# Optimization experiments

Hardware: AMD Instinct MI355X
Metric: run time of the kernel (lower is better)

## Reference

```python
import jax, jax.numpy as jnp
import numpy as np

B, GH, GW, DIM, NH = 1, 48, 64, 1536, 16
HD = DIM // NH          # 96
C = HD // 2             # 48, divisible by 3 as the rope split requires
L = max(GH, GW)


def setup_inputs() -> dict:
    key = jax.random.key(0)
    ks = jax.random.split(key, 6)
    x = jax.random.normal(ks[0], (B, GH * GW, DIM), jnp.float32)
    w_init = lambda k: jax.random.normal(k, (DIM, DIM), jnp.float32) * 0.02
    # rope frequency table: theta[p, j] = p / 10000^(j/C); freqs = exp(i*theta)
    pos = jnp.arange(L, dtype=jnp.float32)[:, None]
    inv = 10000.0 ** (-jnp.arange(C, dtype=jnp.float32) / C)
    theta = pos * inv[None, :]
    return {
        "x": x,
        "wq": w_init(ks[1]), "bq": jnp.zeros((DIM,), jnp.float32),
        "wk": w_init(ks[2]), "bk": jnp.zeros((DIM,), jnp.float32),
        "wv": w_init(ks[3]), "bv": jnp.zeros((DIM,), jnp.float32),
        "wo": w_init(ks[4]), "bo": jnp.zeros((DIM,), jnp.float32),
        "freqs_cos": jnp.cos(theta), "freqs_sin": jnp.sin(theta),
        "h": GH, "w": GW,
    }


def rope_apply_spatial(x, freqs_cos, freqs_sin, h, w):
    # x: [b, s, n, d] with s == h*w. Complex rotation done in real arithmetic.
    b, s, n, d = x.shape
    c = d // 2
    c3 = c // 3
    # channel groups: [0:c3] identity (ones), [c3:2c3] rotated by h-position,
    # [2c3:3c3] rotated by w-position  (matches freqs.split + cat in torch)
    cos_hw = jnp.concatenate([
        jnp.ones((h, w, c3), x.dtype),
        jnp.broadcast_to(freqs_cos[:h, None, c3:2 * c3], (h, w, c3)),
        jnp.broadcast_to(freqs_cos[None, :w, 2 * c3:3 * c3], (h, w, c3)),
    ], axis=-1).reshape(1, s, 1, c)
    sin_hw = jnp.concatenate([
        jnp.zeros((h, w, c3), x.dtype),
        jnp.broadcast_to(freqs_sin[:h, None, c3:2 * c3], (h, w, c3)),
        jnp.broadcast_to(freqs_sin[None, :w, 2 * c3:3 * c3], (h, w, c3)),
    ], axis=-1).reshape(1, s, 1, c)
    xc = x.reshape(b, s, n, c, 2)
    xr, xi = xc[..., 0], xc[..., 1]
    yr = xr * cos_hw - xi * sin_hw
    yi = xr * sin_hw + xi * cos_hw
    return jnp.stack([yr, yi], axis=-1).reshape(b, s, n, d)


def reference(x, wq, bq, wk, bk, wv, bv, wo, bo, freqs_cos, freqs_sin, h, w):
    b, s, _ = x.shape
    q = (x @ wq + bq).reshape(b, s, NH, HD)
    k = (x @ wk + bk).reshape(b, s, NH, HD)
    v = (x @ wv + bv).reshape(b, s, NH, HD)
    q = rope_apply_spatial(q, freqs_cos, freqs_sin, h, w)
    k = rope_apply_spatial(k, freqs_cos, freqs_sin, h, w)
    scale = 1.0 / jnp.sqrt(jnp.asarray(HD, q.dtype))
    scores = jnp.einsum('bqnd,bknd->bnqk', q, k) * scale  # [b, n, s, s]
    attn = jax.nn.softmax(scores, axis=-1)
    out = jnp.einsum('bnqk,bknd->bqnd', attn, v).reshape(b, s, NH * HD)
    return out @ wo + bo
```

## Files before the change

kernel.cpp:

```cpp
#include <hip/hip_runtime.h>
#include <math.h>

#define S_LEN 3072
#define DIM 1536
#define NHEADS 16
#define HDIM 96
#define NPAIR 48

typedef __attribute__((ext_vector_type(8))) _Float16 half8;
typedef __attribute__((ext_vector_type(4))) _Float16 half4v;
typedef __attribute__((ext_vector_type(2))) _Float16 half2v;
typedef __attribute__((ext_vector_type(4))) float f32x4;

__device__ inline void gload16(const void* g, void* l) {
    __builtin_amdgcn_global_load_lds(
        (const __attribute__((address_space(1))) void*)g,
        (__attribute__((address_space(3))) void*)l, 16, 0, 0);
}

__device__ inline uint4 gld128(const _Float16* p) {
    uint4 r;
    asm volatile("global_load_dwordx4 %0, %1, off"
                 : "=v"(r) : "v"(p));
    return r;
}

__global__ __launch_bounds__(256)
void convert_f32_f16(const float* __restrict__ src, _Float16* __restrict__ dst, int n4)
{
    int i = blockIdx.x * 256 + threadIdx.x;
    if (i < n4) {
        float4 v = *(const float4*)&src[(size_t)i * 4];
        half4v h = { (_Float16)v.x, (_Float16)v.y, (_Float16)v.z, (_Float16)v.w };
        *(half4v*)&dst[(size_t)i * 4] = h;
    }
}

__global__ __launch_bounds__(256)
void transpose_w(const float* __restrict__ w0, const float* __restrict__ w1,
                 const float* __restrict__ w2, const float* __restrict__ w3,
                 _Float16* __restrict__ wt)
{
    __shared__ _Float16 t[64][68];
    const int z = blockIdx.z;
    const float* W = (z == 0) ? w0 : (z == 1) ? w1 : (z == 2) ? w2 : w3;
    _Float16* O = wt + (size_t)z * DIM * DIM;
    const int k0 = blockIdx.y * 64, n0 = blockIdx.x * 64;
    const int tid = threadIdx.x;
    const int r = tid >> 4, c4 = (tid & 15) * 4;
#pragma unroll
    for (int g = 0; g < 4; g++) {
        int kk = r + g * 16;
        float4 v = *(const float4*)&W[(size_t)(k0 + kk) * DIM + n0 + c4];
        t[c4 + 0][kk] = (_Float16)v.x; t[c4 + 1][kk] = (_Float16)v.y;
        t[c4 + 2][kk] = (_Float16)v.z; t[c4 + 3][kk] = (_Float16)v.w;
    }
    __syncthreads();
    const int nr = tid >> 2, ks = (tid & 3) * 16;
#pragma unroll
    for (int s = 0; s < 4; s++)
        *(ushort4*)&O[(size_t)(n0 + nr) * DIM + k0 + ks + s * 4] =
            *(ushort4*)&t[nr][ks + s * 4];
}

template<bool QKV>
__global__ __launch_bounds__(256)
void gemm_f16(const _Float16* __restrict__ X,
              const _Float16* __restrict__ W0t, const _Float16* __restrict__ W1t,
              const _Float16* __restrict__ W2t,
              const float* __restrict__ B0, const float* __restrict__ B1,
              const float* __restrict__ B2,
              const float* __restrict__ fc, const float* __restrict__ fs,
              void* __restrict__ outv)
{
    __shared__ __align__(16) _Float16 As[128][64];
    __shared__ __align__(16) _Float16 Bs[128][64];

    const int tid = threadIdx.x;
    const int w = tid >> 6, lane = tid & 63;
    const int ln = lane & 15, quad = lane >> 4;
    const int bz = blockIdx.z;
    const _Float16* Wt = W0t; const float* bias = B0;
    if (QKV) { if (bz == 1) { Wt = W1t; bias = B1; } else if (bz == 2) { Wt = W2t; bias = B2; } }
    const int m0 = blockIdx.y * 128, n0 = blockIdx.x * 128;
    const int wm = w >> 1, wn = w & 1;
    const int row8 = lane >> 3, cch = lane & 7;
    const int gch = cch ^ row8;

    f32x4 acc[4][4];
#pragma unroll
    for (int i = 0; i < 4; i++)
#pragma unroll
        for (int j = 0; j < 4; j++) acc[i][j] = (f32x4){0.f, 0.f, 0.f, 0.f};

    for (int k0 = 0; k0 < DIM; k0 += 64) {
        __syncthreads();
#pragma unroll
        for (int j = 0; j < 4; j++) {
            const int r = w * 32 + j * 8;
            gload16(X  + (size_t)(m0 + r + row8) * DIM + k0 + gch * 8, &As[r][0]);
            gload16(Wt + (size_t)(n0 + r + row8) * DIM + k0 + gch * 8, &Bs[r][0]);
        }
        __syncthreads();

        half8 a[4][2], b[4][2];
#pragma unroll
        for (int mt = 0; mt < 4; mt++) {
            int m = wm * 64 + mt * 16 + ln;
#pragma unroll
            for (int ks = 0; ks < 2; ks++) {
                int s = (ks * 4 + quad) ^ (ln & 7);
                a[mt][ks] = *(const half8*)&As[m][s * 8];
            }
        }
#pragma unroll
        for (int nt = 0; nt < 4; nt++) {
            int n = wn * 64 + nt * 16 + ln;
#pragma unroll
            for (int ks = 0; ks < 2; ks++) {
                int s = (ks * 4 + quad) ^ (ln & 7);
                b[nt][ks] = *(const half8*)&Bs[n][s * 8];
            }
        }
#pragma unroll
        for (int ks = 0; ks < 2; ks++)
#pragma unroll
            for (int mt = 0; mt < 4; mt++)
#pragma unroll
                for (int nt = 0; nt < 4; nt++)
                    acc[mt][nt] = __builtin_amdgcn_mfma_f32_16x16x32_f16(
                        a[mt][ks], b[nt][ks], acc[mt][nt], 0, 0, 0);
    }

#pragma unroll
    for (int nt = 0; nt < 4; nt++) {
        int col = n0 + wn * 64 + nt * 16 + ln;
        float bv = bias[col];
        int head = col / HDIM, hd = col % HDIM;
        int jc = hd >> 1;
        bool isreal = (ln & 1) == 0;
#pragma unroll
        for (int mt = 0; mt < 4; mt++) {
            int row0 = m0 + wm * 64 + mt * 16 + quad * 4;
            if (QKV && bz == 2) {
                half4v p;
#pragma unroll
                for (int r = 0; r < 4; r++) p[r] = (_Float16)(acc[mt][nt][r] + bv);
                *(half4v*)&((_Float16*)outv)[(((size_t)2 * NHEADS + head) * HDIM + hd) * S_LEN + row0] = p;
            } else if (QKV) {
                float v[4], vp[4];
#pragma unroll
                for (int r = 0; r < 4; r++) v[r] = acc[mt][nt][r] + bv;
#pragma unroll
                for (int r = 0; r < 4; r++) vp[r] = __shfl_xor(v[r], 1);
#pragma unroll
                for (int r = 0; r < 4; r++) {
                    int srow = row0 + r;
                    int pos = (jc < 32) ? (srow >> 6) : (srow & 63);
                    float c  = fc[pos * NPAIR + jc];
                    float sn = fs[pos * NPAIR + jc];
                    float xr = isreal ? v[r] : vp[r];
                    float xi = isreal ? vp[r] : v[r];
                    float rot = isreal ? (xr * c - xi * sn) : (xr * sn + xi * c);
                    float outval = (jc < 16) ? v[r] : rot;
                    ((_Float16*)outv)[(((size_t)bz * NHEADS + head) * S_LEN + srow) * HDIM + hd]
                        = (_Float16)outval;
                }
            } else {
#pragma unroll
                for (int r = 0; r < 4; r++)
                    ((float*)outv)[(size_t)(row0 + r) * DIM + col] = acc[mt][nt][r] + bv;
            }
        }
    }
}

__global__ __launch_bounds__(256, 2)
void attn_mfma_kernel(const _Float16* __restrict__ qh, const _Float16* __restrict__ kh,
                      const _Float16* __restrict__ vtg, _Float16* __restrict__ aoh)
{
    __shared__ __align__(16) _Float16 Kb[2][2][64 * 96];
    __shared__ __align__(16) _Float16 Vt[2][96][72];

    const int tid  = threadIdx.x;
    const int wid  = tid >> 6;
    const int p    = wid >> 1;
    const int wp   = wid & 1;
    const int lane = tid & 63;
    const int ln   = lane & 15;
    const int quad = lane >> 4;
    const int h    = blockIdx.y;
    const int q0   = blockIdx.x * 64;
    const float scale_ = 0.10206207261596577f * 1.4426950408889634f;
    const int NT = (S_LEN / 2) / 64;

    half8 aq[2][3];
#pragma unroll
    for (int qs = 0; qs < 2; qs++) {
        const _Float16* qrow = qh + (((size_t)h * S_LEN) + q0 + (wp * 2 + qs) * 16 + ln) * HDIM;
#pragma unroll
        for (int kb = 0; kb < 3; kb++) {
            half8 a = *(const half8*)&qrow[kb * 32 + quad * 8];
            half8 v;
#pragma unroll
            for (int i = 0; i < 8; i++) v[i] = (_Float16)((float)a[i] * scale_);
            aq[qs][kb] = v;
        }
    }

    f32x4 o[2][6];
#pragma unroll
    for (int qs = 0; qs < 2; qs++)
#pragma unroll
        for (int dn = 0; dn < 6; dn++) o[qs][dn] = (f32x4){0.f, 0.f, 0.f, 0.f};
    float m_[2] = {-INFINITY, -INFINITY}, l_[2] = {0.f, 0.f};

    const char* kbase = (const char*)(kh + ((size_t)h * S_LEN + p * (S_LEN / 2)) * HDIM);

    int koffb[6];
#pragma unroll
    for (int i = 0; i < 6; i++) {
        int pc = i * 128 + (tid & 127);
        int r  = pc / 12, c = pc - r * 12;
        int rm = r % 12;
        int cl = c - rm; if (cl < 0) cl += 12;
        koffb[i] = r * 192 + cl * 16;
    }
    const int A0 = (quad + ln) % 12;
    int ksel[3];
    ksel[0] = A0 * 16;
    { int t1 = A0 + 4; if (t1 >= 12) t1 -= 12; ksel[1] = t1 * 16; }
    { int t2 = A0 + 8; if (t2 >= 12) t2 -= 12; ksel[2] = t2 * 16; }

    const int tp = tid & 127;
    const int vd0 = tp >> 3, vc = tp & 7;
    const _Float16* vsrc0 = vtg + (size_t)h * HDIM * S_LEN + (size_t)vd0 * S_LEN
                          + p * (S_LEN / 2) + vc * 8;
    _Float16* vdst = &Vt[p][vd0][(vc ^ (vd0 & 7)) * 8];

#pragma unroll
    for (int i = 0; i < 6; i++)
        gload16(kbase + koffb[i], &Kb[p][0][i * 1024 + wp * 512]);
    uint4 vp0, vp1, vp2, vp3, vp4, vp5;
    vp0 = gld128(vsrc0 + 0 * 16 * S_LEN);
    vp1 = gld128(vsrc0 + 1 * 16 * S_LEN);
    vp2 = gld128(vsrc0 + 2 * 16 * S_LEN);
    vp3 = gld128(vsrc0 + 3 * 16 * S_LEN);
    vp4 = gld128(vsrc0 + 4 * 16 * S_LEN);
    vp5 = gld128(vsrc0 + 5 * 16 * S_LEN);
    asm volatile("s_waitcnt vmcnt(0)" ::: "memory");
    __builtin_amdgcn_sched_barrier(0);
    *(uint4*)(vdst + 0 * 16 * 72) = vp0;  *(uint4*)(vdst + 1 * 16 * 72) = vp1;
    *(uint4*)(vdst + 2 * 16 * 72) = vp2;  *(uint4*)(vdst + 3 * 16 * 72) = vp3;
    *(uint4*)(vdst + 4 * 16 * 72) = vp4;  *(uint4*)(vdst + 5 * 16 * 72) = vp5;
    __syncthreads();

    for (int kt = 0; kt < NT; ++kt) {
        const int cur = kt & 1;
        if (kt + 1 < NT) {
            const char* ks2 = kbase + (size_t)(kt + 1) * 12288;
#pragma unroll
            for (int i = 0; i < 6; i++)
                gload16(ks2 + koffb[i], &Kb[p][cur ^ 1][i * 1024 + wp * 512]);
            const _Float16* vs2 = vsrc0 + (kt + 1) * 64;
            vp0 = gld128(vs2 + 0 * 16 * S_LEN);
            vp1 = gld128(vs2 + 1 * 16 * S_LEN);
            vp2 = gld128(vs2 + 2 * 16 * S_LEN);
            vp3 = gld128(vs2 + 3 * 16 * S_LEN);
            vp4 = gld128(vs2 + 4 * 16 * S_LEN);
            vp5 = gld128(vs2 + 5 * 16 * S_LEN);
            __builtin_amdgcn_sched_barrier(0);
        }

        const char* Kc = (const char*)&Kb[p][cur][0];
        f32x4 s[2][4];
#pragma unroll
        for (int nb = 0; nb < 4; nb++) {
            const char* krow = Kc + (nb * 16 + ln) * 192;
            half8 ak0 = *(const half8*)(krow + ksel[(nb + 0) % 3]);
            half8 ak1 = *(const half8*)(krow + ksel[(nb + 1) % 3]);
            half8 ak2 = *(const half8*)(krow + ksel[(nb + 2) % 3]);
#pragma unroll
            for (int qs = 0; qs < 2; qs++) {
                f32x4 acc = (f32x4){0.f, 0.f, 0.f, 0.f};
                acc = __builtin_amdgcn_mfma_f32_16x16x32_f16(ak0, aq[qs][0], acc, 0, 0, 0);
                acc = __builtin_amdgcn_mfma_f32_16x16x32_f16(ak1, aq[qs][1], acc, 0, 0, 0);
                acc = __builtin_amdgcn_mfma_f32_16x16x32_f16(ak2, aq[qs][2], acc, 0, 0, 0);
                s[qs][nb] = acc;
            }
        }

        half4v ap[2][4];
#pragma unroll
        for (int qs = 0; qs < 2; qs++) {
            float ma = fmaxf(fmaxf(s[qs][0][0], s[qs][0][1]), fmaxf(s[qs][0][2], s[qs][0][3]));
            float mb = fmaxf(fmaxf(s[qs][1][0], s[qs][1][1]), fmaxf(s[qs][1][2], s[qs][1][3]));
            float mc = fmaxf(fmaxf(s[qs][2][0], s[qs][2][1]), fmaxf(s[qs][2][2], s[qs][2][3]));
            float md = fmaxf(fmaxf(s[qs][3][0], s[qs][3][1]), fmaxf(s[qs][3][2], s[qs][3][3]));
            float mx = fmaxf(fmaxf(ma, mb), fmaxf(mc, md));
            if (!__all(mx <= m_[qs] + 8.0f)) {
                mx = fmaxf(mx, __shfl_xor(mx, 16));
                mx = fmaxf(mx, __shfl_xor(mx, 32));
                float mn = fmaxf(m_[qs], mx);
                float al = __builtin_amdgcn_exp2f(m_[qs] - mn);
                m_[qs] = mn;
                l_[qs] *= al;
#pragma unroll
                for (int dn = 0; dn < 6; dn++)
#pragma unroll
                    for (int r = 0; r < 4; r++) o[qs][dn][r] *= al;
            }
            float rs = 0.f;
            float mq = m_[qs];
#pragma unroll
            for (int nb = 0; nb < 4; nb++) {
                float p0 = __builtin_amdgcn_exp2f(s[qs][nb][0] - mq);
                float p1 = __builtin_amdgcn_exp2f(s[qs][nb][1] - mq);
                float p2 = __builtin_amdgcn_exp2f(s[qs][nb][2] - mq);
                float p3 = __builtin_amdgcn_exp2f(s[qs][nb][3] - mq);
                rs += (p0 + p1) + (p2 + p3);
                half4v pk = { (_Float16)p0, (_Float16)p1, (_Float16)p2, (_Float16)p3 };
                ap[qs][nb] = pk;
            }
            l_[qs] += rs;
        }

#pragma unroll
        for (int nb = 0; nb < 4; nb++) {
            const int off = (((nb * 2 + (quad >> 1)) ^ (ln & 7)) * 8) + (quad & 1) * 4;
#pragma unroll
            for (int dn = 0; dn < 6; dn++) {
                half4v av = *(const half4v*)&Vt[p][dn * 16 + ln][off];
                o[0][dn] = __builtin_amdgcn_mfma_f32_16x16x16f16(av, ap[0][nb], o[0][dn], 0, 0, 0);
                o[1][dn] = __builtin_amdgcn_mfma_f32_16x16x16f16(av, ap[1][nb], o[1][dn], 0, 0, 0);
            }
        }

        __syncthreads();
        asm volatile("s_waitcnt vmcnt(0)" ::: "memory");
        __builtin_amdgcn_sched_barrier(0);
        if (kt + 1 < NT) {
            *(uint4*)(vdst + 0 * 16 * 72) = vp0;  *(uint4*)(vdst + 1 * 16 * 72) = vp1;
            *(uint4*)(vdst + 2 * 16 * 72) = vp2;  *(uint4*)(vdst + 3 * 16 * 72) = vp3;
            *(uint4*)(vdst + 4 * 16 * 72) = vp4;  *(uint4*)(vdst + 5 * 16 * 72) = vp5;
        }
        __syncthreads();
    }

    float lt[2];
#pragma unroll
    for (int qs = 0; qs < 2; qs++) {
        float l = l_[qs];
        l += __shfl_xor(l, 16);
        l += __shfl_xor(l, 32);
        lt[qs] = l;
    }
    float*  scr = (float*)&Kb[0][0][0];
    float2* mlb = (float2*)((char*)&Kb[0][0][0] + 26624);
    if (p == 1) {
#pragma unroll
        for (int qs = 0; qs < 2; qs++) {
            int row = (wp * 2 + qs) * 16 + ln;
            if (quad == 0) mlb[row] = make_float2(m_[qs], lt[qs]);
#pragma unroll
            for (int dn = 0; dn < 6; dn++)
                *(f32x4*)&scr[row * 100 + dn * 16 + quad * 4] = o[qs][dn];
        }
    }
    __syncthreads();
    if (p == 0) {
#pragma unroll
        for (int qs = 0; qs < 2; qs++) {
            int row = (wp * 2 + qs) * 16 + ln;
            float2 ml1 = mlb[row];
            float mm = fmaxf(m_[qs], ml1.x);
            float a0 = __builtin_amdgcn_exp2f(m_[qs] - mm);
            float a1 = __builtin_amdgcn_exp2f(ml1.x - mm);
            float li = 1.0f / (lt[qs] * a0 + ml1.y * a1);
            const size_t rowbase = (size_t)(q0 + row) * DIM + h * HDIM;
#pragma unroll
            for (int dn = 0; dn < 6; dn++) {
                f32x4 o1 = *(const f32x4*)&scr[row * 100 + dn * 16 + quad * 4];
                half4v pk;
#pragma unroll
                for (int r = 0; r < 4; r++)
                    pk[r] = (_Float16)((o[qs][dn][r] * a0 + o1[r] * a1) * li);
                *(half4v*)&aoh[rowbase + dn * 16 + quad * 4] = pk;
            }
        }
    }
}

extern "C" void kernel_launch(void* const* d_in, const int* in_sizes, int n_in,
                              void* d_out, int out_size, void* d_ws, size_t ws_size,
                              hipStream_t stream) {
    const float* x  = (const float*)d_in[0];
    const float* wq = (const float*)d_in[1];
    const float* bq = (const float*)d_in[2];
    const float* wk = (const float*)d_in[3];
    const float* bk = (const float*)d_in[4];
    const float* wv = (const float*)d_in[5];
    const float* bv = (const float*)d_in[6];
    const float* wo = (const float*)d_in[7];
    const float* bo = (const float*)d_in[8];
    const float* fc = (const float*)d_in[9];
    const float* fs = (const float*)d_in[10];
    float* out = (float*)d_out;

    const size_t per  = (size_t)NHEADS * S_LEN * HDIM;
    const size_t dim2 = (size_t)DIM * DIM;
    _Float16* hws  = (_Float16*)d_ws;
    _Float16* qkvh = hws;
    _Float16* qh   = qkvh;
    _Float16* kh   = qkvh + per;
    _Float16* vth  = qkvh + 2 * per;
    _Float16* xh   = hws + 3 * per;
    _Float16* wth  = hws + 4 * per;

    convert_f32_f16<<<(int)((S_LEN * DIM / 4 + 255) / 256), 256, 0, stream>>>(
        x, xh, S_LEN * DIM / 4);
    transpose_w<<<dim3(DIM / 64, DIM / 64, 4), 256, 0, stream>>>(wq, wk, wv, wo, wth);

    gemm_f16<true><<<dim3(DIM / 128, S_LEN / 128, 3), 256, 0, stream>>>(
        xh, wth, wth + dim2, wth + 2 * dim2, bq, bk, bv, fc, fs, qkvh);
    attn_mfma_kernel<<<dim3(S_LEN / 64, NHEADS), 256, 0, stream>>>(qh, kh, vth, xh);
    gemm_f16<false><<<dim3(DIM / 128, S_LEN / 128, 1), 256, 0, stream>>>(
        xh, wth + 3 * dim2, nullptr, nullptr, bo, nullptr, nullptr, fc, fs, out);
}
```

Baseline: 333.3 us.

## Switch attention kernel to 32x32 MFMA tiles with one query block per wave

Each wave now owns a single 32-row query tile and uses 32x32x16 MFMAs for QK^T and 32x32x8 MFMAs for PV, in place of 16x16 tiles over two query sub-blocks. The K and V LDS read addressing and swizzles are recomputed for the new operand layouts, and V's row pitch shrinks from 72 to 64, relying on the XOR swizzle to avoid bank conflicts. The aim is fewer MFMA issues and fewer LDS fragment reads per key tile. In exchange, accumulator pressure rises (three f32x16 outputs plus two f32x16 score tiles), which may affect occupancy at the two-blocks-per-SM launch bound.

```diff
diff --git a/kernel.cpp b/kernel.cpp
--- a/kernel.cpp
+++ b/kernel.cpp
@@ -11,6 +11,7 @@
 typedef __attribute__((ext_vector_type(4))) _Float16 half4v;
 typedef __attribute__((ext_vector_type(2))) _Float16 half2v;
 typedef __attribute__((ext_vector_type(4))) float f32x4;
+typedef __attribute__((ext_vector_type(16))) float f32x16;
 
 __device__ inline void gload16(const void* g, void* l) {
     __builtin_amdgcn_global_load_lds(
@@ -180,40 +181,39 @@
                       const _Float16* __restrict__ vtg, _Float16* __restrict__ aoh)
 {
     __shared__ __align__(16) _Float16 Kb[2][2][64 * 96];
-    __shared__ __align__(16) _Float16 Vt[2][96][72];
+    __shared__ __align__(16) _Float16 Vt[2][96][64];
 
     const int tid  = threadIdx.x;
     const int wid  = tid >> 6;
     const int p    = wid >> 1;
     const int wp   = wid & 1;
     const int lane = tid & 63;
-    const int ln   = lane & 15;
-    const int quad = lane >> 4;
+    const int rloc = lane & 31;
+    const int hi   = lane >> 5;
+    const int r7   = rloc & 7;
+    const int hi4  = hi * 4;
     const int h    = blockIdx.y;
     const int q0   = blockIdx.x * 64;
     const float scale_ = 0.10206207261596577f * 1.4426950408889634f;
     const int NT = (S_LEN / 2) / 64;
 
-    half8 aq[2][3];
-#pragma unroll
-    for (int qs = 0; qs < 2; qs++) {
-        const _Float16* qrow = qh + (((size_t)h * S_LEN) + q0 + (wp * 2 + qs) * 16 + ln) * HDIM;
-#pragma unroll
-        for (int kb = 0; kb < 3; kb++) {
-            half8 a = *(const half8*)&qrow[kb * 32 + quad * 8];
-            half8 v;
-#pragma unroll
-            for (int i = 0; i < 8; i++) v[i] = (_Float16)((float)a[i] * scale_);
-            aq[qs][kb] = v;
-        }
-    }
-
-    f32x4 o[2][6];
-#pragma unroll
-    for (int qs = 0; qs < 2; qs++)
-#pragma unroll
-        for (int dn = 0; dn < 6; dn++) o[qs][dn] = (f32x4){0.f, 0.f, 0.f, 0.f};
-    float m_[2] = {-INFINITY, -INFINITY}, l_[2] = {0.f, 0.f};
+    const _Float16* qrow = qh + (((size_t)h * S_LEN) + q0 + wp * 32 + rloc) * HDIM;
+    half8 aq[6];
+#pragma unroll
+    for (int kc = 0; kc < 6; kc++) {
+        half8 a = *(const half8*)&qrow[kc * 16 + 8 * hi];
+        half8 v;
+#pragma unroll
+        for (int i = 0; i < 8; i++) v[i] = (_Float16)((float)a[i] * scale_);
+        aq[kc] = v;
+    }
+
+    f32x16 o32[3];
+#pragma unroll
+    for (int d = 0; d < 3; d++)
+#pragma unroll
+        for (int i = 0; i < 16; i++) o32[d][i] = 0.f;
+    float m_ = -INFINITY, l_ = 0.f;
 
     const char* kbase = (const char*)(kh + ((size_t)h * S_LEN + p * (S_LEN / 2)) * HDIM);
 
@@ -226,11 +226,14 @@
         int cl = c - rm; if (cl < 0) cl += 12;
         koffb[i] = r * 192 + cl * 16;
     }
-    const int A0 = (quad + ln) % 12;
-    int ksel[3];
-    ksel[0] = A0 * 16;
-    { int t1 = A0 + 4; if (t1 >= 12) t1 -= 12; ksel[1] = t1 * 16; }
-    { int t2 = A0 + 8; if (t2 >= 12) t2 -= 12; ksel[2] = t2 * 16; }
+    int koffA[6], koffB[6];
+#pragma unroll
+    for (int kc = 0; kc < 6; kc++) {
+        int rA = rloc,      pA = (hi + 2 * kc + rA) % 12;
+        int rB = 32 + rloc, pB = (hi + 2 * kc + rB) % 12;
+        koffA[kc] = rA * 192 + pA * 16;
+        koffB[kc] = rB * 192 + pB * 16;
+    }
 
     const int tp = tid & 127;
     const int vd0 = tp >> 3, vc = tp & 7;
@@ -250,9 +253,9 @@
     vp5 = gld128(vsrc0 + 5 * 16 * S_LEN);
     asm volatile("s_waitcnt vmcnt(0)" ::: "memory");
     __builtin_amdgcn_sched_barrier(0);
-    *(uint4*)(vdst + 0 * 16 * 72) = vp0;  *(uint4*)(vdst + 1 * 16 * 72) = vp1;
-    *(uint4*)(vdst + 2 * 16 * 72) = vp2;  *(uint4*)(vdst + 3 * 16 * 72) = vp3;
-    *(uint4*)(vdst + 4 * 16 * 72) = vp4;  *(uint4*)(vdst + 5 * 16 * 72) = vp5;
+    *(uint4*)(vdst + 0 * 16 * 64) = vp0;  *(uint4*)(vdst + 1 * 16 * 64) = vp1;
+    *(uint4*)(vdst + 2 * 16 * 64) = vp2;  *(uint4*)(vdst + 3 * 16 * 64) = vp3;
+    *(uint4*)(vdst + 4 * 16 * 64) = vp4;  *(uint4*)(vdst + 5 * 16 * 64) = vp5;
     __syncthreads();
 
     for (int kt = 0; kt < NT; ++kt) {
@@ -273,66 +276,62 @@
         }
 
         const char* Kc = (const char*)&Kb[p][cur][0];
-        f32x4 s[2][4];
-#pragma unroll
-        for (int nb = 0; nb < 4; nb++) {
-            const char* krow = Kc + (nb * 16 + ln) * 192;
-            half8 ak0 = *(const half8*)(krow + ksel[(nb + 0) % 3]);
-            half8 ak1 = *(const half8*)(krow + ksel[(nb + 1) % 3]);
-            half8 ak2 = *(const half8*)(krow + ksel[(nb + 2) % 3]);
-#pragma unroll
-            for (int qs = 0; qs < 2; qs++) {
-                f32x4 acc = (f32x4){0.f, 0.f, 0.f, 0.f};
-                acc = __builtin_amdgcn_mfma_f32_16x16x32_f16(ak0, aq[qs][0], acc, 0, 0, 0);
-                acc = __builtin_amdgcn_mfma_f32_16x16x32_f16(ak1, aq[qs][1], acc, 0, 0, 0);
-                acc = __builtin_amdgcn_mfma_f32_16x16x32_f16(ak2, aq[qs][2], acc, 0, 0, 0);
-                s[qs][nb] = acc;
-            }
-        }
-
-        half4v ap[2][4];
-#pragma unroll
-        for (int qs = 0; qs < 2; qs++) {
-            float ma = fmaxf(fmaxf(s[qs][0][0], s[qs][0][1]), fmaxf(s[qs][0][2], s[qs][0][3]));
-            float mb = fmaxf(fmaxf(s[qs][1][0], s[qs][1][1]), fmaxf(s[qs][1][2], s[qs][1][3]));
-            float mc = fmaxf(fmaxf(s[qs][2][0], s[qs][2][1]), fmaxf(s[qs][2][2], s[qs][2][3]));
-            float md = fmaxf(fmaxf(s[qs][3][0], s[qs][3][1]), fmaxf(s[qs][3][2], s[qs][3][3]));
-            float mx = fmaxf(fmaxf(ma, mb), fmaxf(mc, md));
-            if (!__all(mx <= m_[qs] + 8.0f)) {
-                mx = fmaxf(mx, __shfl_xor(mx, 16));
-                mx = fmaxf(mx, __shfl_xor(mx, 32));
-                float mn = fmaxf(m_[qs], mx);
-                float al = __builtin_amdgcn_exp2f(m_[qs] - mn);
-                m_[qs] = mn;
-                l_[qs] *= al;
-#pragma unroll
-                for (int dn = 0; dn < 6; dn++)
-#pragma unroll
-                    for (int r = 0; r < 4; r++) o[qs][dn][r] *= al;
-            }
-            float rs = 0.f;
-            float mq = m_[qs];
-#pragma unroll
-            for (int nb = 0; nb < 4; nb++) {
-                float p0 = __builtin_amdgcn_exp2f(s[qs][nb][0] - mq);
-                float p1 = __builtin_amdgcn_exp2f(s[qs][nb][1] - mq);
-                float p2 = __builtin_amdgcn_exp2f(s[qs][nb][2] - mq);
-                float p3 = __builtin_amdgcn_exp2f(s[qs][nb][3] - mq);
-                rs += (p0 + p1) + (p2 + p3);
-                half4v pk = { (_Float16)p0, (_Float16)p1, (_Float16)p2, (_Float16)p3 };
-                ap[qs][nb] = pk;
-            }
-            l_[qs] += rs;
-        }
-
-#pragma unroll
-        for (int nb = 0; nb < 4; nb++) {
-            const int off = (((nb * 2 + (quad >> 1)) ^ (ln & 7)) * 8) + (quad & 1) * 4;
-#pragma unroll
-            for (int dn = 0; dn < 6; dn++) {
-                half4v av = *(const half4v*)&Vt[p][dn * 16 + ln][off];
-                o[0][dn] = __builtin_amdgcn_mfma_f32_16x16x16f16(av, ap[0][nb], o[0][dn], 0, 0, 0);
-                o[1][dn] = __builtin_amdgcn_mfma_f32_16x16x16f16(av, ap[1][nb], o[1][dn], 0, 0, 0);
+        f32x16 sA, sB;
+#pragma unroll
+        for (int i = 0; i < 16; i++) { sA[i] = 0.f; sB[i] = 0.f; }
+#pragma unroll
+        for (int kc = 0; kc < 6; kc++) {
+            half8 ka = *(const half8*)(Kc + koffA[kc]);
+            half8 kb = *(const half8*)(Kc + koffB[kc]);
+            sA = __builtin_amdgcn_mfma_f32_32x32x16_f16(ka, aq[kc], sA, 0, 0, 0);
+            sB = __builtin_amdgcn_mfma_f32_32x32x16_f16(kb, aq[kc], sB, 0, 0, 0);
+        }
+
+        float mx = sA[0];
+#pragma unroll
+        for (int i = 1; i < 16; i++) mx = fmaxf(mx, sA[i]);
+#pragma unroll
+        for (int i = 0; i < 16; i++) mx = fmaxf(mx, sB[i]);
+        if (!__all(mx <= m_ + 8.0f)) {
+            mx = fmaxf(mx, __shfl_xor(mx, 32));
+            float mn = fmaxf(m_, mx);
+            float al = __builtin_amdgcn_exp2f(m_ - mn);
+            m_ = mn; l_ *= al;
+#pragma unroll
+            for (int d = 0; d < 3; d++)
+#pragma unroll
+                for (int i = 0; i < 16; i++) o32[d][i] *= al;
+        }
+        float rs = 0.f;
+#pragma unroll
+        for (int i = 0; i < 16; i++) {
+            float e = __builtin_amdgcn_exp2f(sA[i] - m_); sA[i] = e; rs += e;
+        }
+#pragma unroll
+        for (int i = 0; i < 16; i++) {
+            float e = __builtin_amdgcn_exp2f(sB[i] - m_); sB[i] = e; rs += e;
+        }
+        l_ += rs;
+
+        half4v pf[8];
+#pragma unroll
+        for (int t = 0; t < 4; t++) {
+            half4v v0, v1;
+            v0[0] = (_Float16)sA[4 * t + 0]; v0[1] = (_Float16)sA[4 * t + 1];
+            v0[2] = (_Float16)sA[4 * t + 2]; v0[3] = (_Float16)sA[4 * t + 3];
+            v1[0] = (_Float16)sB[4 * t + 0]; v1[1] = (_Float16)sB[4 * t + 1];
+            v1[2] = (_Float16)sB[4 * t + 2]; v1[3] = (_Float16)sB[4 * t + 3];
+            pf[t]     = v0;
+            pf[4 + t] = v1;
+        }
+
+#pragma unroll
+        for (int nb8 = 0; nb8 < 8; nb8++) {
+            const int co = ((nb8 ^ r7) << 3) + hi4;
+#pragma unroll
+            for (int d = 0; d < 3; d++) {
+                half4v av = *(const half4v*)&Vt[p][d * 32 + rloc][co];
+                o32[d] = __builtin_amdgcn_mfma_f32_32x32x8f16(av, pf[nb8], o32[d], 0, 0, 0);
             }
         }
 
@@ -340,54 +339,47 @@
         asm volatile("s_waitcnt vmcnt(0)" ::: "memory");
         __builtin_amdgcn_sched_barrier(0);
         if (kt + 1 < NT) {
-            *(uint4*)(vdst + 0 * 16 * 72) = vp0;  *(uint4*)(vdst + 1 * 16 * 72) = vp1;
-            *(uint4*)(vdst + 2 * 16 * 72) = vp2;  *(uint4*)(vdst + 3 * 16 * 72) = vp3;
-            *(uint4*)(vdst + 4 * 16 * 72) = vp4;  *(uint4*)(vdst + 5 * 16 * 72) = vp5;
+            *(uint4*)(vdst + 0 * 16 * 64) = vp0;  *(uint4*)(vdst + 1 * 16 * 64) = vp1;
+            *(uint4*)(vdst + 2 * 16 * 64) = vp2;  *(uint4*)(vdst + 3 * 16 * 64) = vp3;
+            *(uint4*)(vdst + 4 * 16 * 64) = vp4;  *(uint4*)(vdst + 5 * 16 * 64) = vp5;
         }
         __syncthreads();
     }
 
-    float lt[2];
-#pragma unroll
-    for (int qs = 0; qs < 2; qs++) {
-        float l = l_[qs];
-        l += __shfl_xor(l, 16);
-        l += __shfl_xor(l, 32);
-        lt[qs] = l;
-    }
+    const float lt = l_ + __shfl_xor(l_, 32);
+    const int qrl = wp * 32 + rloc;
     float*  scr = (float*)&Kb[0][0][0];
     float2* mlb = (float2*)((char*)&Kb[0][0][0] + 26624);
     if (p == 1) {
-#pragma unroll
-        for (int qs = 0; qs < 2; qs++) {
-            int row = (wp * 2 + qs) * 16 + ln;
-            if (quad == 0) mlb[row] = make_float2(m_[qs], lt[qs]);
-#pragma unroll
-            for (int dn = 0; dn < 6; dn++)
-                *(f32x4*)&scr[row * 100 + dn * 16 + quad * 4] = o[qs][dn];
-        }
+        if (hi == 0) mlb[qrl] = make_float2(m_, lt);
+#pragma unroll
+        for (int d = 0; d < 3; d++)
+#pragma unroll
+            for (int b2 = 0; b2 < 4; b2++) {
+                f32x4 c4 = { o32[d][4 * b2 + 0], o32[d][4 * b2 + 1],
+                             o32[d][4 * b2 + 2], o32[d][4 * b2 + 3] };
+                *(f32x4*)&scr[qrl * 100 + d * 32 + 8 * b2 + hi4] = c4;
+            }
     }
     __syncthreads();
     if (p == 0) {
-#pragma unroll
-        for (int qs = 0; qs < 2; qs++) {
-            int row = (wp * 2 + qs) * 16 + ln;
-            float2 ml1 = mlb[row];
-            float mm = fmaxf(m_[qs], ml1.x);
-            float a0 = __builtin_amdgcn_exp2f(m_[qs] - mm);
-            float a1 = __builtin_amdgcn_exp2f(ml1.x - mm);
-            float li = 1.0f / (lt[qs] * a0 + ml1.y * a1);
-            const size_t rowbase = (size_t)(q0 + row) * DIM + h * HDIM;
-#pragma unroll
-            for (int dn = 0; dn < 6; dn++) {
-                f32x4 o1 = *(const f32x4*)&scr[row * 100 + dn * 16 + quad * 4];
+        float2 ml1 = mlb[qrl];
+        float mm = fmaxf(m_, ml1.x);
+        float a0 = __builtin_amdgcn_exp2f(m_ - mm);
+        float a1 = __builtin_amdgcn_exp2f(ml1.x - mm);
+        float li = 1.0f / (lt * a0 + ml1.y * a1);
+        const size_t rowbase = (size_t)(q0 + qrl) * DIM + h * HDIM;
+#pragma unroll
+        for (int d = 0; d < 3; d++)
+#pragma unroll
+            for (int b2 = 0; b2 < 4; b2++) {
+                f32x4 o1 = *(const f32x4*)&scr[qrl * 100 + d * 32 + 8 * b2 + hi4];
                 half4v pk;
 #pragma unroll
                 for (int r = 0; r < 4; r++)
-                    pk[r] = (_Float16)((o[qs][dn][r] * a0 + o1[r] * a1) * li);
-                *(half4v*)&aoh[rowbase + dn * 16 + quad * 4] = pk;
-            }
-        }
+                    pk[r] = (_Float16)((o32[d][4 * b2 + r] * a0 + o1[r] * a1) * li);
+                *(half4v*)&aoh[rowbase + d * 32 + 8 * b2 + hi4] = pk;
+            }
     }
 }
 
```

After: 330.5 us. No clear change (-0.8%).

## Use 256x256 double-buffered GEMM tiles with 512-thread blocks for projections

Applied to the files above, without the earlier changes.

Replaces the 128x128 projection GEMM with a 256x256 tile computed by 8 waves, each owning a 128x64 sub-tile. The next K-slice is prefetched into a second LDS buffer while the current one is multiplied, so global loads overlap with MFMA work and each element loaded is reused more. The cost is fewer blocks: 216 for the fused QKV projection and only 72 for the output projection, which leaves many CUs idle. The kernel also uses about 128 KB of LDS and pins occupancy to one block per CU.

```diff
diff --git a/kernel.cpp b/kernel.cpp
--- a/kernel.cpp
+++ b/kernel.cpp
@@ -64,17 +64,17 @@
 }
 
 template<bool QKV>
-__global__ __launch_bounds__(256)
-void gemm_f16(const _Float16* __restrict__ X,
-              const _Float16* __restrict__ W0t, const _Float16* __restrict__ W1t,
-              const _Float16* __restrict__ W2t,
-              const float* __restrict__ B0, const float* __restrict__ B1,
-              const float* __restrict__ B2,
-              const float* __restrict__ fc, const float* __restrict__ fs,
-              void* __restrict__ outv)
+__global__ __launch_bounds__(512, 1)
+void gemm256_f16(const _Float16* __restrict__ X,
+                 const _Float16* __restrict__ W0t, const _Float16* __restrict__ W1t,
+                 const _Float16* __restrict__ W2t,
+                 const float* __restrict__ B0, const float* __restrict__ B1,
+                 const float* __restrict__ B2,
+                 const float* __restrict__ fc, const float* __restrict__ fs,
+                 void* __restrict__ outv)
 {
-    __shared__ __align__(16) _Float16 As[128][64];
-    __shared__ __align__(16) _Float16 Bs[128][64];
+    __shared__ __align__(16) _Float16 AsB[2][256 * 64];
+    __shared__ __align__(16) _Float16 BsB[2][256 * 64];
 
     const int tid = threadIdx.x;
     const int w = tid >> 6, lane = tid & 63;
@@ -82,54 +82,59 @@
     const int bz = blockIdx.z;
     const _Float16* Wt = W0t; const float* bias = B0;
     if (QKV) { if (bz == 1) { Wt = W1t; bias = B1; } else if (bz == 2) { Wt = W2t; bias = B2; } }
-    const int m0 = blockIdx.y * 128, n0 = blockIdx.x * 128;
-    const int wm = w >> 1, wn = w & 1;
-    const int row8 = lane >> 3, cch = lane & 7;
-    const int gch = cch ^ row8;
-
-    f32x4 acc[4][4];
-#pragma unroll
-    for (int i = 0; i < 4; i++)
+    const int m0 = blockIdx.y * 256, n0 = blockIdx.x * 256;
+    const int wm = w >> 2, wn = w & 3;
+    const int row8 = lane >> 3, gch = (lane & 7) ^ row8;
+
+    f32x4 acc[8][4];
+#pragma unroll
+    for (int i = 0; i < 8; i++)
 #pragma unroll
         for (int j = 0; j < 4; j++) acc[i][j] = (f32x4){0.f, 0.f, 0.f, 0.f};
 
-    for (int k0 = 0; k0 < DIM; k0 += 64) {
-        __syncthreads();
-#pragma unroll
-        for (int j = 0; j < 4; j++) {
-            const int r = w * 32 + j * 8;
-            gload16(X  + (size_t)(m0 + r + row8) * DIM + k0 + gch * 8, &As[r][0]);
-            gload16(Wt + (size_t)(n0 + r + row8) * DIM + k0 + gch * 8, &Bs[r][0]);
-        }
-        __syncthreads();
-
-        half8 a[4][2], b[4][2];
-#pragma unroll
-        for (int mt = 0; mt < 4; mt++) {
-            int m = wm * 64 + mt * 16 + ln;
-#pragma unroll
-            for (int ks = 0; ks < 2; ks++) {
-                int s = (ks * 4 + quad) ^ (ln & 7);
-                a[mt][ks] = *(const half8*)&As[m][s * 8];
-            }
-        }
-#pragma unroll
-        for (int nt = 0; nt < 4; nt++) {
-            int n = wn * 64 + nt * 16 + ln;
-#pragma unroll
-            for (int ks = 0; ks < 2; ks++) {
-                int s = (ks * 4 + quad) ^ (ln & 7);
-                b[nt][ks] = *(const half8*)&Bs[n][s * 8];
-            }
-        }
-#pragma unroll
-        for (int ks = 0; ks < 2; ks++)
-#pragma unroll
-            for (int mt = 0; mt < 4; mt++)
+#pragma unroll
+    for (int j = 0; j < 4; j++) {
+        const int r = w * 32 + j * 8;
+        gload16(X  + (size_t)(m0 + r + row8) * DIM + 0 + gch * 8, &AsB[0][r * 64]);
+        gload16(Wt + (size_t)(n0 + r + row8) * DIM + 0 + gch * 8, &BsB[0][r * 64]);
+    }
+    asm volatile("s_waitcnt vmcnt(0)");
+    __syncthreads();
+
+    const int NKT = DIM / 64;
+    for (int kt = 0; kt < NKT; ++kt) {
+        const int cur = kt & 1;
+        if (kt + 1 < NKT) {
+            const int k0 = (kt + 1) * 64;
+#pragma unroll
+            for (int j = 0; j < 4; j++) {
+                const int r = w * 32 + j * 8;
+                gload16(X  + (size_t)(m0 + r + row8) * DIM + k0 + gch * 8, &AsB[cur ^ 1][r * 64]);
+                gload16(Wt + (size_t)(n0 + r + row8) * DIM + k0 + gch * 8, &BsB[cur ^ 1][r * 64]);
+            }
+            __builtin_amdgcn_sched_barrier(0);
+        }
+
+#pragma unroll
+        for (int ks = 0; ks < 2; ks++) {
+            const int s8 = (((ks * 4 + quad) ^ (ln & 7))) * 8;
+            half8 a[8], b[4];
+#pragma unroll
+            for (int mt = 0; mt < 8; mt++)
+                a[mt] = *(const half8*)&AsB[cur][(wm * 128 + mt * 16 + ln) * 64 + s8];
+#pragma unroll
+            for (int nt = 0; nt < 4; nt++)
+                b[nt] = *(const half8*)&BsB[cur][(wn * 64 + nt * 16 + ln) * 64 + s8];
+#pragma unroll
+            for (int mt = 0; mt < 8; mt++)
 #pragma unroll
                 for (int nt = 0; nt < 4; nt++)
                     acc[mt][nt] = __builtin_amdgcn_mfma_f32_16x16x32_f16(
-                        a[mt][ks], b[nt][ks], acc[mt][nt], 0, 0, 0);
+                        a[mt], b[nt], acc[mt][nt], 0, 0, 0);
+        }
+
+        asm volatile("s_waitcnt vmcnt(0)");
+        __syncthreads();
     }
 
 #pragma unroll
@@ -140,8 +145,8 @@
         int jc = hd >> 1;
         bool isreal = (ln & 1) == 0;
 #pragma unroll
-        for (int mt = 0; mt < 4; mt++) {
-            int row0 = m0 + wm * 64 + mt * 16 + quad * 4;
+        for (int mt = 0; mt < 8; mt++) {
+            int row0 = m0 + wm * 128 + mt * 16 + quad * 4;
             if (QKV && bz == 2) {
                 half4v p;
 #pragma unroll
@@ -421,9 +426,9 @@
         x, xh, S_LEN * DIM / 4);
     transpose_w<<<dim3(DIM / 64, DIM / 64, 4), 256, 0, stream>>>(wq, wk, wv, wo, wth);
 
-    gemm_f16<true><<<dim3(DIM / 128, S_LEN / 128, 3), 256, 0, stream>>>(
+    gemm256_f16<true><<<dim3(DIM / 256, S_LEN / 256, 3), 512, 0, stream>>>(
         xh, wth, wth + dim2, wth + 2 * dim2, bq, bk, bv, fc, fs, qkvh);
     attn_mfma_kernel<<<dim3(S_LEN / 64, NHEADS), 256, 0, stream>>>(qh, kh, vth, xh);
-    gemm_f16<false><<<dim3(DIM / 128, S_LEN / 128, 1), 256, 0, stream>>>(
+    gemm256_f16<false><<<dim3(DIM / 256, S_LEN / 256, 1), 512, 0, stream>>>(
         xh, wth + 3 * dim2, nullptr, nullptr, bo, nullptr, nullptr, fc, fs, out);
 }
```

Result: no change. 335.5 us (+0.7%).
